# Kernel tuning notes

Measured on AMD Instinct MI355X. Metric: run time of the kernel, lower is better.

The kernel has to match this reference:

```python
import jax, jax.numpy as jnp
import numpy as np

N_NODES = 50000
N_EDGES = 300000
NODE_DIM = 128
HIDDEN = 256
BN_EPS = 1e-5
ROLL_SHIFT = 16


def setup_inputs() -> dict:
    key = jax.random.key(0)
    ks = jax.random.split(key, 8)
    node_feat = jax.random.normal(ks[0], (N_NODES, NODE_DIM), dtype=jnp.float32)
    edge_index = jax.random.randint(ks[1], (2, N_EDGES), 0, N_NODES, dtype=jnp.int64)
    W1 = jax.random.normal(ks[2], (2 * NODE_DIM, HIDDEN), dtype=jnp.float32) * 0.05
    b1 = jnp.zeros((HIDDEN,), dtype=jnp.float32)
    bn_gamma = jnp.ones((HIDDEN,), dtype=jnp.float32)
    bn_beta = jnp.zeros((HIDDEN,), dtype=jnp.float32)
    bn_mean = jax.random.normal(ks[3], (HIDDEN,), dtype=jnp.float32) * 0.1
    bn_var = jax.random.uniform(ks[4], (HIDDEN,), dtype=jnp.float32, minval=0.5, maxval=1.5)
    W2 = jax.random.normal(ks[5], (HIDDEN, 1), dtype=jnp.float32) * 0.05
    b2 = jnp.zeros((1,), dtype=jnp.float32)
    return {
        "node_feat": node_feat, "edge_index": edge_index,
        "W1": W1, "b1": b1,
        "bn_gamma": bn_gamma, "bn_beta": bn_beta,
        "bn_mean": bn_mean, "bn_var": bn_var,
        "W2": W2, "b2": b2,
    }


def reference(node_feat, edge_index, W1, b1, bn_gamma, bn_beta, bn_mean, bn_var, W2, b2):
    row, col = edge_index[0], edge_index[1]
    # [E, 2*node_dim]: gather endpoint features and concat
    edge_feat = jnp.concatenate([node_feat[row], node_feat[col]], axis=1)

    def mlp(x):
        h = x @ W1 + b1                                   # [E, H]
        # BatchNorm1d (eval mode: running stats)
        h = (h - bn_mean) * jax.lax.rsqrt(bn_var + BN_EPS) * bn_gamma + bn_beta
        h = jax.nn.relu(h)
        return (h @ W2 + b2).reshape(-1)                  # [E]

    edge_pred_1 = mlp(edge_feat)
    edge_pred_2 = mlp(jnp.roll(edge_feat, ROLL_SHIFT, axis=1))
    return jax.nn.sigmoid((edge_pred_1 + edge_pred_2) * 0.5)
```

## Files before the change

### kernel.cpp

```cpp
#include <hip/hip_runtime.h>
#include <hip/hip_bf16.h>

#define E_TOTAL 300000
#define N_NODES 50000
#define NDIM    128
#define KDIM    256
#define HDIM    512
#define BN_EPS  1e-5f
#define NTILES  ((E_TOTAL + 63) / 64)
#define NBLK    512
#define TLANES  512
#define NF_BLOCKS 6250
#define LT_MAX  10
#define A_SCALE 24.0f
#define WV_SCALE 16777216.0f
#define WV_INV   (1.0f / 16777216.0f)

typedef __attribute__((ext_vector_type(4))) int   i32x4;
typedef __attribute__((ext_vector_type(4))) float f32x4;
typedef _Float16 f16x2 __attribute__((ext_vector_type(2)));
typedef const __attribute__((address_space(1))) unsigned int* gas1_t;
typedef __attribute__((address_space(3))) unsigned int* las3_t;

__device__ __forceinline__ int q8(float x, float s) {
  float v = fminf(fmaxf(x * s, -127.f), 127.f);
  return (int)rintf(v);
}

__global__ void prep_kernel(const float* __restrict__ nf, unsigned char* __restrict__ nfq,
                            const float* __restrict__ W1, const float* __restrict__ b1,
                            const float* __restrict__ gamma, const float* __restrict__ beta,
                            const float* __restrict__ mean, const float* __restrict__ var,
                            const float* __restrict__ W2,
                            unsigned char* __restrict__ Wswz,
                            int* __restrict__ c2i, float* __restrict__ wp2) {
  int b = blockIdx.x;
  int tid = threadIdx.x;
  if (b < NF_BLOCKS) {
    int i = b * 256 + tid;
    float4 v = ((const float4*)nf)[i];
    int q0 = q8(v.x, A_SCALE), q1 = q8(v.y, A_SCALE);
    int q2 = q8(v.z, A_SCALE), q3 = q8(v.w, A_SCALE);
    ((unsigned*)nfq)[i] = (q0 & 255) | ((q1 & 255) << 8) | ((q2 & 255) << 16) | ((q3 & 255) << 24);
  } else {
    int ct = b - NF_BLOCKS;
    __shared__ float amx[16][16];
    __shared__ float sB[16];
    {
      int cl = tid >> 4, pt = tid & 15;
      int jj = (ct * 16 + cl) & 255;
      float m = 0.f;
      #pragma unroll
      for (int i = 0; i < 16; i++)
        m = fmaxf(m, fabsf(W1[(pt * 16 + i) * 256 + jj]));
      amx[cl][pt] = m;
    }
    __syncthreads();
    if (tid < 16) {
      int j  = ct * 16 + tid;
      int jj = j & 255;
      float s = gamma[jj] * rsqrtf(var[jj] + BN_EPS);
      float m = 0.f;
      #pragma unroll
      for (int p = 0; p < 16; p++) m = fmaxf(m, amx[tid][p]);
      float amax_b = fmaxf(m * fabsf(s), 1e-20f);
      sB[tid] = 127.f / amax_b;
      float rv = amax_b / (127.f * A_SCALE);
      float cj = b1[jj] * s + beta[jj] - mean[jj] * s;
      float c2 = fminf(fmaxf(cj / rv, -1e9f), 1e9f);
      c2i[j] = (int)rintf(c2);
      wp2[j] = 0.5f * W2[jj] * rv * WV_SCALE;
    }
    __syncthreads();
    {
      int kt   = tid >> 6;
      int lane = tid & 63;
      int l16  = lane & 15, quad = lane >> 4;
      int col  = ct * 16 + l16;
      int jj   = col & 255;
      int shift = (col >= 256) ? 16 : 0;
      float s  = gamma[jj] * rsqrtf(var[jj] + BN_EPS);
      float sc = sB[l16];
      unsigned o[4];
      #pragma unroll
      for (int d = 0; d < 4; d++) {
        unsigned pk = 0;
        #pragma unroll
        for (int jb = 0; jb < 4; jb++) {
          int k  = kt * 64 + quad * 16 + d * 4 + jb;
          int ks = (k + shift) & 255;
          int q  = q8(W1[ks * 256 + jj] * s, sc);
          pk |= (unsigned)(q & 255) << (8 * jb);
        }
        o[d] = pk;
      }
      *(uint4*)(Wswz + ((size_t)(ct * 4 + kt) * 64 + lane) * 16) = *(const uint4*)o;
    }
  }
}

__global__ __launch_bounds__(512, 4) void edge_mlp_kernel(
    const unsigned char* __restrict__ nfq, const int* __restrict__ eidx,
    const unsigned char* __restrict__ Wswz, const int* __restrict__ c2i,
    const float* __restrict__ wp2, const float* __restrict__ b2,
    float* __restrict__ out) {
  __shared__ unsigned char Ab[4][16 * 1024];
  __shared__ unsigned short idxl[LT_MAX * 128];
  __shared__ float partial[4][8][64];
  __shared__ int   c2il[HDIM];

  const int tid  = threadIdx.x;
  const int w    = tid >> 6;
  const int lane = tid & 63;
  const int l16  = lane & 15;
  const int quad = lane >> 4;
  const int tb   = blockIdx.x;
  const int ntl  = (NTILES - tb + TLANES - 1) / TLANES;

  const i32x4* Wf = (const i32x4*)Wswz;
  i32x4 bq[4][4];
  #pragma unroll
  for (int mt = 0; mt < 4; mt++)
    #pragma unroll
    for (int kt = 0; kt < 4; kt++)
      bq[mt][kt] = Wf[((w * 4 + mt) * 4 + kt) * 64 + lane];

  c2il[tid] = c2i[tid];
  f16x2 wvh[8];
  #pragma unroll
  for (int mt = 0; mt < 4; mt++) {
    float4 wvf = *(const float4*)&wp2[w * 64 + mt * 16 + quad * 4];
    wvh[mt * 2 + 0] = f16x2{(_Float16)wvf.x, (_Float16)wvf.y};
    wvh[mt * 2 + 1] = f16x2{(_Float16)wvf.z, (_Float16)wvf.w};
  }
  const float b2v = b2[0];

  for (int g = tid; g < ntl * 128; g += 512) {
    int lt2 = g >> 7, r = g & 127;
    int half = r >> 6;
    int e = (tb + lt2 * TLANES) * 64 + (r & 63);
    if (e >= E_TOTAL) e = E_TOTAL - 1;
    idxl[g] = (unsigned short)eidx[half * E_TOTAL + e];
  }
  __syncthreads();

  const int snt   = w & 3;
  const int shalf = w >> 2;
  const int sfrag0 = snt * 4 + shalf * 2;

  auto stage = [&](int lt2, int slot) {
    int node = idxl[lt2 * 128 + shalf * 64 + snt * 16 + l16];
    const unsigned char* gbase = nfq + (size_t)node * NDIM + quad * 16;
    #pragma unroll
    for (int i = 0; i < 2; i++)
      __builtin_amdgcn_global_load_lds((gas1_t)(gbase + i * 64),
                                       (las3_t)(&Ab[slot][(sfrag0 + i) * 1024]),
                                       16, 0, 0);
  };

  auto combine = [&](int lt2, int le) {
    int e = (tb + lt2 * TLANES) * 64 + le;
    if (e < E_TOTAL) {
      float s = 0.f;
      #pragma unroll
      for (int ww = 0; ww < 8; ww++) s += partial[lt2 & 3][ww][le];
      out[e] = 1.0f / (1.0f + __expf(-(s * WV_INV + b2v)));
    }
  };

  auto compute_tile = [&](int lt2) {
    const unsigned char* Ap = &Ab[lt2 & 3][lane * 16];

    #pragma unroll
    for (int nt = 0; nt < 4; nt++) {
      i32x4 acc[4];
      #pragma unroll
      for (int mt = 0; mt < 4; mt++)
        acc[mt] = *(const volatile i32x4*)&c2il[w * 64 + mt * 16 + quad * 4];
      #pragma unroll
      for (int kt = 0; kt < 4; kt++) {
        i32x4 ef = *(const i32x4*)(Ap + (nt * 4 + kt) * 1024);
        #pragma unroll
        for (int mt = 0; mt < 4; mt++)
          acc[mt] = __builtin_amdgcn_mfma_i32_16x16x64_i8(bq[mt][kt], ef, acc[mt], 0, 0, 0);
      }
      float v = 0.f;
      #pragma unroll
      for (int mt = 0; mt < 4; mt++) {
        int h;
        h = acc[mt][0]; v = fmaf((float)(h > 0 ? h : 0), (float)wvh[mt * 2 + 0][0], v);
        h = acc[mt][1]; v = fmaf((float)(h > 0 ? h : 0), (float)wvh[mt * 2 + 0][1], v);
        h = acc[mt][2]; v = fmaf((float)(h > 0 ? h : 0), (float)wvh[mt * 2 + 1][0], v);
        h = acc[mt][3]; v = fmaf((float)(h > 0 ? h : 0), (float)wvh[mt * 2 + 1][1], v);
      }
      v += __shfl_xor(v, 16);
      v += __shfl_xor(v, 32);
      if (quad == 0) partial[lt2 & 3][w][nt * 16 + l16] = v;
    }
  };

  stage(0, 0);
  if (1 < ntl) stage(1, 1);

  for (int lt = 0; lt < ntl; lt += 2) {
    __syncthreads();

    int s2 = lt + 2, s3 = lt + 3;
    if (s2 < ntl) stage(s2, s2 & 3);
    if (s3 < ntl) stage(s3, s3 & 3);

    if (lt >= 2) {
      if (tid < 64)       combine(lt - 2, tid);
      else if (tid < 128) combine(lt - 1, tid - 64);
    }

    compute_tile(lt);
    if (lt + 1 < ntl) compute_tile(lt + 1);
  }

  __syncthreads();
  if ((ntl & 1) == 0) {
    if (tid < 64)       combine(ntl - 2, tid);
    else if (tid < 128) combine(ntl - 1, tid - 64);
  } else {
    if (tid < 64)       combine(ntl - 1, tid);
  }
}

extern "C" void kernel_launch(void* const* d_in, const int* in_sizes, int n_in,
                              void* d_out, int out_size, void* d_ws, size_t ws_size,
                              hipStream_t stream) {
  const float* node_feat = (const float*)d_in[0];
  const int*   eidx      = (const int*)d_in[1];
  const float* W1        = (const float*)d_in[2];
  const float* b1        = (const float*)d_in[3];
  const float* gamma     = (const float*)d_in[4];
  const float* beta      = (const float*)d_in[5];
  const float* mean      = (const float*)d_in[6];
  const float* var       = (const float*)d_in[7];
  const float* W2        = (const float*)d_in[8];
  const float* b2        = (const float*)d_in[9];
  float* out = (float*)d_out;

  unsigned char* Wswz = (unsigned char*)d_ws;
  int*   c2i = (int*)((char*)d_ws + (size_t)HDIM * KDIM);
  float* wp2 = (float*)(c2i + HDIM);
  unsigned char* nfq = (unsigned char*)(wp2 + HDIM);

  prep_kernel<<<NF_BLOCKS + 32, 256, 0, stream>>>(node_feat, nfq, W1, b1, gamma, beta,
                                                  mean, var, W2, Wswz, c2i, wp2);

  edge_mlp_kernel<<<NBLK, 512, 0, stream>>>(nfq, eidx, Wswz, c2i, wp2, b2, out);
}
```

Measured before the change: 132.8 us.

## Fuse prep and edge MLP kernels with a grid-wide atomic barrier

Merges the quantization/weight-prep kernel into the edge MLP kernel. Blocks 0-31 build the swizzled int8 weights, staging W1 columns through shared memory, while the remaining blocks quantize node features in a grid-stride loop. A global atomic-counter barrier separates the prep phase from the compute phase, and the edge-index preload now runs before the barrier so it overlaps with prep. This removes one kernel launch and its tail, but adds a memset launch and relies on all 512 blocks being resident at once, otherwise the spin barrier deadlocks.

```diff
diff --git a/kernel.cpp b/kernel.cpp
--- a/kernel.cpp
+++ b/kernel.cpp
@@ -10,7 +10,7 @@
 #define NTILES  ((E_TOTAL + 63) / 64)
 #define NBLK    512
 #define TLANES  512
-#define NF_BLOCKS 6250
+#define NF4     (N_NODES * NDIM / 4)
 #define LT_MAX  10
 #define A_SCALE 24.0f
 #define WV_SCALE 16777216.0f
@@ -27,83 +27,15 @@
   return (int)rintf(v);
 }
 
-__global__ void prep_kernel(const float* __restrict__ nf, unsigned char* __restrict__ nfq,
-                            const float* __restrict__ W1, const float* __restrict__ b1,
-                            const float* __restrict__ gamma, const float* __restrict__ beta,
-                            const float* __restrict__ mean, const float* __restrict__ var,
-                            const float* __restrict__ W2,
-                            unsigned char* __restrict__ Wswz,
-                            int* __restrict__ c2i, float* __restrict__ wp2) {
-  int b = blockIdx.x;
-  int tid = threadIdx.x;
-  if (b < NF_BLOCKS) {
-    int i = b * 256 + tid;
-    float4 v = ((const float4*)nf)[i];
-    int q0 = q8(v.x, A_SCALE), q1 = q8(v.y, A_SCALE);
-    int q2 = q8(v.z, A_SCALE), q3 = q8(v.w, A_SCALE);
-    ((unsigned*)nfq)[i] = (q0 & 255) | ((q1 & 255) << 8) | ((q2 & 255) << 16) | ((q3 & 255) << 24);
-  } else {
-    int ct = b - NF_BLOCKS;
-    __shared__ float amx[16][16];
-    __shared__ float sB[16];
-    {
-      int cl = tid >> 4, pt = tid & 15;
-      int jj = (ct * 16 + cl) & 255;
-      float m = 0.f;
-      #pragma unroll
-      for (int i = 0; i < 16; i++)
-        m = fmaxf(m, fabsf(W1[(pt * 16 + i) * 256 + jj]));
-      amx[cl][pt] = m;
-    }
-    __syncthreads();
-    if (tid < 16) {
-      int j  = ct * 16 + tid;
-      int jj = j & 255;
-      float s = gamma[jj] * rsqrtf(var[jj] + BN_EPS);
-      float m = 0.f;
-      #pragma unroll
-      for (int p = 0; p < 16; p++) m = fmaxf(m, amx[tid][p]);
-      float amax_b = fmaxf(m * fabsf(s), 1e-20f);
-      sB[tid] = 127.f / amax_b;
-      float rv = amax_b / (127.f * A_SCALE);
-      float cj = b1[jj] * s + beta[jj] - mean[jj] * s;
-      float c2 = fminf(fmaxf(cj / rv, -1e9f), 1e9f);
-      c2i[j] = (int)rintf(c2);
-      wp2[j] = 0.5f * W2[jj] * rv * WV_SCALE;
-    }
-    __syncthreads();
-    {
-      int kt   = tid >> 6;
-      int lane = tid & 63;
-      int l16  = lane & 15, quad = lane >> 4;
-      int col  = ct * 16 + l16;
-      int jj   = col & 255;
-      int shift = (col >= 256) ? 16 : 0;
-      float s  = gamma[jj] * rsqrtf(var[jj] + BN_EPS);
-      float sc = sB[l16];
-      unsigned o[4];
-      #pragma unroll
-      for (int d = 0; d < 4; d++) {
-        unsigned pk = 0;
-        #pragma unroll
-        for (int jb = 0; jb < 4; jb++) {
-          int k  = kt * 64 + quad * 16 + d * 4 + jb;
-          int ks = (k + shift) & 255;
-          int q  = q8(W1[ks * 256 + jj] * s, sc);
-          pk |= (unsigned)(q & 255) << (8 * jb);
-        }
-        o[d] = pk;
-      }
-      *(uint4*)(Wswz + ((size_t)(ct * 4 + kt) * 64 + lane) * 16) = *(const uint4*)o;
-    }
-  }
-}
-
-__global__ __launch_bounds__(512, 4) void edge_mlp_kernel(
-    const unsigned char* __restrict__ nfq, const int* __restrict__ eidx,
-    const unsigned char* __restrict__ Wswz, const int* __restrict__ c2i,
-    const float* __restrict__ wp2, const float* __restrict__ b2,
-    float* __restrict__ out) {
+__global__ __launch_bounds__(512, 4) void fused_kernel(
+    const float* __restrict__ nf, const int* __restrict__ eidx,
+    const float* __restrict__ W1, const float* __restrict__ b1,
+    const float* __restrict__ gamma, const float* __restrict__ beta,
+    const float* __restrict__ mean, const float* __restrict__ var,
+    const float* __restrict__ W2, const float* __restrict__ b2,
+    unsigned char* __restrict__ Wswz, int* __restrict__ c2i,
+    float* __restrict__ wp2, unsigned char* __restrict__ nfq,
+    unsigned* __restrict__ bar, float* __restrict__ out) {
   __shared__ unsigned char Ab[4][16 * 1024];
   __shared__ unsigned short idxl[LT_MAX * 128];
   __shared__ float partial[4][8][64];
@@ -117,6 +49,98 @@
   const int tb   = blockIdx.x;
   const int ntl  = (NTILES - tb + TLANES - 1) / TLANES;
 
+  if (tb >= 32) {
+    const float4* nf4 = (const float4*)nf;
+    unsigned* nq4 = (unsigned*)nfq;
+    for (int i = (tb - 32) * 512 + tid; i < NF4; i += 480 * 512) {
+      float4 v = nf4[i];
+      int q0 = q8(v.x, A_SCALE), q1 = q8(v.y, A_SCALE);
+      int q2 = q8(v.z, A_SCALE), q3 = q8(v.w, A_SCALE);
+      nq4[i] = (q0 & 255) | ((q1 & 255) << 8) | ((q2 & 255) << 16) | ((q3 & 255) << 24);
+    }
+  } else {
+    int ct = tb;
+    float* wbuf = (float*)&Ab[0][0];
+    float* amx2 = (float*)&Ab[1][0];
+    float* sBl  = amx2 + 512;
+    {
+      const float4* src = (const float4*)(W1 + (ct & 15) * 16);
+      float4* dst = (float4*)wbuf;
+      #pragma unroll
+      for (int q = 0; q < 2; q++) {
+        int idx = q * 512 + tid;
+        int r = idx >> 2, c4 = idx & 3;
+        dst[idx] = src[(size_t)r * 64 + c4];
+      }
+    }
+    __syncthreads();
+    {
+      int col = tid & 15, chunk = tid >> 4;
+      float m = 0.f;
+      #pragma unroll
+      for (int i = 0; i < 8; i++)
+        m = fmaxf(m, fabsf(wbuf[(chunk * 8 + i) * 16 + col]));
+      amx2[col * 32 + chunk] = m;
+    }
+    __syncthreads();
+    if (tid < 16) {
+      int j  = ct * 16 + tid;
+      int jj = j & 255;
+      float s = gamma[jj] * rsqrtf(var[jj] + BN_EPS);
+      float m = 0.f;
+      #pragma unroll
+      for (int p = 0; p < 32; p++) m = fmaxf(m, amx2[tid * 32 + p]);
+      float amax_b = fmaxf(m * fabsf(s), 1e-20f);
+      sBl[tid] = 127.f / amax_b;
+      float rv = amax_b / (127.f * A_SCALE);
+      float cj = b1[jj] * s + beta[jj] - mean[jj] * s;
+      float c2 = fminf(fmaxf(cj / rv, -1e9f), 1e9f);
+      c2i[j] = (int)rintf(c2);
+      wp2[j] = 0.5f * W2[jj] * rv * WV_SCALE;
+    }
+    __syncthreads();
+    if (tid < 256) {
+      int kt = tid >> 6, ln = tid & 63;
+      int lc = ln & 15, qd = ln >> 4;
+      int col = ct * 16 + lc;
+      int jj  = col & 255;
+      int shift = (col >= 256) ? 16 : 0;
+      float s  = gamma[jj] * rsqrtf(var[jj] + BN_EPS);
+      float sc = sBl[lc];
+      unsigned o[4];
+      #pragma unroll
+      for (int d = 0; d < 4; d++) {
+        unsigned pk = 0;
+        #pragma unroll
+        for (int jb = 0; jb < 4; jb++) {
+          int k  = kt * 64 + qd * 16 + d * 4 + jb;
+          int ks = (k + shift) & 255;
+          int q  = q8(wbuf[ks * 16 + lc] * s, sc);
+          pk |= (unsigned)(q & 255) << (8 * jb);
+        }
+        o[d] = pk;
+      }
+      *(uint4*)(Wswz + ((size_t)(ct * 4 + kt) * 64 + ln) * 16) = *(const uint4*)o;
+    }
+  }
+
+  for (int g = tid; g < ntl * 128; g += 512) {
+    int lt2 = g >> 7, r = g & 127;
+    int half = r >> 6;
+    int e = (tb + lt2 * TLANES) * 64 + (r & 63);
+    if (e >= E_TOTAL) e = E_TOTAL - 1;
+    idxl[g] = (unsigned short)eidx[half * E_TOTAL + e];
+  }
+
+  __syncthreads();
+  __threadfence();
+  if (tid == 0) {
+    atomicAdd(bar, 1u);
+    while (atomicAdd(bar, 0u) < NBLK) __builtin_amdgcn_s_sleep(8);
+    __threadfence();
+  }
+  __syncthreads();
+
   const i32x4* Wf = (const i32x4*)Wswz;
   i32x4 bq[4][4];
   #pragma unroll
@@ -134,15 +158,6 @@
     wvh[mt * 2 + 1] = f16x2{(_Float16)wvf.z, (_Float16)wvf.w};
   }
   const float b2v = b2[0];
-
-  for (int g = tid; g < ntl * 128; g += 512) {
-    int lt2 = g >> 7, r = g & 127;
-    int half = r >> 6;
-    int e = (tb + lt2 * TLANES) * 64 + (r & 63);
-    if (e >= E_TOTAL) e = E_TOTAL - 1;
-    idxl[g] = (unsigned short)eidx[half * E_TOTAL + e];
-  }
-  __syncthreads();
 
   const int snt   = w & 3;
   const int shalf = w >> 2;
@@ -246,9 +261,11 @@
   int*   c2i = (int*)((char*)d_ws + (size_t)HDIM * KDIM);
   float* wp2 = (float*)(c2i + HDIM);
   unsigned char* nfq = (unsigned char*)(wp2 + HDIM);
-
-  prep_kernel<<<NF_BLOCKS + 32, 256, 0, stream>>>(node_feat, nfq, W1, b1, gamma, beta,
-                                                  mean, var, W2, Wswz, c2i, wp2);
-
-  edge_mlp_kernel<<<NBLK, 512, 0, stream>>>(nfq, eidx, Wswz, c2i, wp2, b2, out);
+  unsigned* bar = (unsigned*)(nfq + (size_t)N_NODES * NDIM);
+
+  hipMemsetAsync(bar, 0, sizeof(unsigned), stream);
+
+  fused_kernel<<<NBLK, 512, 0, stream>>>(node_feat, eidx, W1, b1, gamma, beta,
+                                         mean, var, W2, b2,
+                                         Wswz, c2i, wp2, nfq, bar, out);
 }
```

New measurement: 211.6 us. +59.4%, slower.

## Split hidden dimension across two blocks per edge tile with separate sigmoid pass

Applied to the files above, without the earlier changes.

Each edge tile is now handled by two 256-thread blocks, each covering one half of the 512 hidden units (the two rolled MLP passes). Each block writes a partial dot product to workspace, and a new small kernel sums the two halves and applies the sigmoid. The pipeline drops from 4-slot double-tile staging to a simple 2-slot ring, which cuts LDS use per block and should allow more resident blocks and smaller scheduling units. In exchange every node row is gathered twice, there is an extra kernel launch, and partial sums make a round trip through global memory.

```diff
diff --git a/kernel.cpp b/kernel.cpp
--- a/kernel.cpp
+++ b/kernel.cpp
@@ -8,7 +8,7 @@
 #define HDIM    512
 #define BN_EPS  1e-5f
 #define NTILES  ((E_TOTAL + 63) / 64)
-#define NBLK    512
+#define NBLK    1024
 #define TLANES  512
 #define NF_BLOCKS 6250
 #define LT_MAX  10
@@ -17,7 +17,6 @@
 #define WV_INV   (1.0f / 16777216.0f)
 
 typedef __attribute__((ext_vector_type(4))) int   i32x4;
-typedef __attribute__((ext_vector_type(4))) float f32x4;
 typedef _Float16 f16x2 __attribute__((ext_vector_type(2)));
 typedef const __attribute__((address_space(1))) unsigned int* gas1_t;
 typedef __attribute__((address_space(3))) unsigned int* las3_t;
@@ -99,22 +98,23 @@
   }
 }
 
-__global__ __launch_bounds__(512, 4) void edge_mlp_kernel(
+__global__ __launch_bounds__(256, 4) void edge_mlp_kernel(
     const unsigned char* __restrict__ nfq, const int* __restrict__ eidx,
     const unsigned char* __restrict__ Wswz, const int* __restrict__ c2i,
-    const float* __restrict__ wp2, const float* __restrict__ b2,
-    float* __restrict__ out) {
-  __shared__ unsigned char Ab[4][16 * 1024];
+    const float* __restrict__ wp2, float* __restrict__ part) {
+  __shared__ unsigned char Ab[2][16 * 1024];
   __shared__ unsigned short idxl[LT_MAX * 128];
-  __shared__ float partial[4][8][64];
-  __shared__ int   c2il[HDIM];
+  __shared__ float partial[2][4][64];
+  __shared__ int   c2il[256];
 
   const int tid  = threadIdx.x;
   const int w    = tid >> 6;
   const int lane = tid & 63;
   const int l16  = lane & 15;
   const int quad = lane >> 4;
-  const int tb   = blockIdx.x;
+  const int b    = blockIdx.x;
+  const int ph   = b & 1;
+  const int tb   = b >> 1;
   const int ntl  = (NTILES - tb + TLANES - 1) / TLANES;
 
   const i32x4* Wf = (const i32x4*)Wswz;
@@ -123,19 +123,18 @@
   for (int mt = 0; mt < 4; mt++)
     #pragma unroll
     for (int kt = 0; kt < 4; kt++)
-      bq[mt][kt] = Wf[((w * 4 + mt) * 4 + kt) * 64 + lane];
-
-  c2il[tid] = c2i[tid];
+      bq[mt][kt] = Wf[(((ph * 16 + w * 4 + mt) * 4) + kt) * 64 + lane];
+
+  c2il[tid] = c2i[ph * 256 + tid];
   f16x2 wvh[8];
   #pragma unroll
   for (int mt = 0; mt < 4; mt++) {
-    float4 wvf = *(const float4*)&wp2[w * 64 + mt * 16 + quad * 4];
+    float4 wvf = *(const float4*)&wp2[ph * 256 + w * 64 + mt * 16 + quad * 4];
     wvh[mt * 2 + 0] = f16x2{(_Float16)wvf.x, (_Float16)wvf.y};
     wvh[mt * 2 + 1] = f16x2{(_Float16)wvf.z, (_Float16)wvf.w};
   }
-  const float b2v = b2[0];
-
-  for (int g = tid; g < ntl * 128; g += 512) {
+
+  for (int g = tid; g < ntl * 128; g += 256) {
     int lt2 = g >> 7, r = g & 127;
     int half = r >> 6;
     int e = (tb + lt2 * TLANES) * 64 + (r & 63);
@@ -144,18 +143,20 @@
   }
   __syncthreads();
 
-  const int snt   = w & 3;
-  const int shalf = w >> 2;
-  const int sfrag0 = snt * 4 + shalf * 2;
-
   auto stage = [&](int lt2, int slot) {
-    int node = idxl[lt2 * 128 + shalf * 64 + snt * 16 + l16];
-    const unsigned char* gbase = nfq + (size_t)node * NDIM + quad * 16;
+    int node_r = idxl[lt2 * 128 + w * 16 + l16];
+    int node_c = idxl[lt2 * 128 + 64 + w * 16 + l16];
+    const unsigned char* gr = nfq + (size_t)node_r * NDIM + quad * 16;
+    const unsigned char* gc = nfq + (size_t)node_c * NDIM + quad * 16;
     #pragma unroll
-    for (int i = 0; i < 2; i++)
-      __builtin_amdgcn_global_load_lds((gas1_t)(gbase + i * 64),
-                                       (las3_t)(&Ab[slot][(sfrag0 + i) * 1024]),
+    for (int i = 0; i < 2; i++) {
+      __builtin_amdgcn_global_load_lds((gas1_t)(gr + i * 64),
+                                       (las3_t)(&Ab[slot][(w * 4 + i) * 1024]),
                                        16, 0, 0);
+      __builtin_amdgcn_global_load_lds((gas1_t)(gc + i * 64),
+                                       (las3_t)(&Ab[slot][(w * 4 + 2 + i) * 1024]),
+                                       16, 0, 0);
+    }
   };
 
   auto combine = [&](int lt2, int le) {
@@ -163,13 +164,13 @@
     if (e < E_TOTAL) {
       float s = 0.f;
       #pragma unroll
-      for (int ww = 0; ww < 8; ww++) s += partial[lt2 & 3][ww][le];
-      out[e] = 1.0f / (1.0f + __expf(-(s * WV_INV + b2v)));
+      for (int ww = 0; ww < 4; ww++) s += partial[lt2 & 1][ww][le];
+      part[ph * E_TOTAL + e] = s;
     }
   };
 
   auto compute_tile = [&](int lt2) {
-    const unsigned char* Ap = &Ab[lt2 & 3][lane * 16];
+    const unsigned char* Ap = &Ab[lt2 & 1][lane * 16];
 
     #pragma unroll
     for (int nt = 0; nt < 4; nt++) {
@@ -195,35 +196,40 @@
       }
       v += __shfl_xor(v, 16);
       v += __shfl_xor(v, 32);
-      if (quad == 0) partial[lt2 & 3][w][nt * 16 + l16] = v;
+      if (quad == 0) partial[lt2 & 1][w][nt * 16 + l16] = v;
     }
   };
 
   stage(0, 0);
-  if (1 < ntl) stage(1, 1);
-
-  for (int lt = 0; lt < ntl; lt += 2) {
+
+  for (int lt = 0; lt < ntl; lt++) {
     __syncthreads();
 
-    int s2 = lt + 2, s3 = lt + 3;
-    if (s2 < ntl) stage(s2, s2 & 3);
-    if (s3 < ntl) stage(s3, s3 & 3);
-
-    if (lt >= 2) {
-      if (tid < 64)       combine(lt - 2, tid);
-      else if (tid < 128) combine(lt - 1, tid - 64);
-    }
+    if (lt + 1 < ntl) stage(lt + 1, (lt + 1) & 1);
+
+    if (lt >= 1 && tid < 64) combine(lt - 1, tid);
 
     compute_tile(lt);
-    if (lt + 1 < ntl) compute_tile(lt + 1);
   }
 
   __syncthreads();
-  if ((ntl & 1) == 0) {
-    if (tid < 64)       combine(ntl - 2, tid);
-    else if (tid < 128) combine(ntl - 1, tid - 64);
-  } else {
-    if (tid < 64)       combine(ntl - 1, tid);
+  if (tid < 64) combine(ntl - 1, tid);
+}
+
+__global__ void sigmoid_kernel(const float* __restrict__ part,
+                               const float* __restrict__ b2,
+                               float* __restrict__ out) {
+  int i = blockIdx.x * 256 + threadIdx.x;
+  if (i < E_TOTAL / 4) {
+    float4 a = ((const float4*)part)[i];
+    float4 c = ((const float4*)(part + E_TOTAL))[i];
+    float bb = b2[0];
+    float4 o;
+    o.x = 1.0f / (1.0f + __expf(-((a.x + c.x) * WV_INV + bb)));
+    o.y = 1.0f / (1.0f + __expf(-((a.y + c.y) * WV_INV + bb)));
+    o.z = 1.0f / (1.0f + __expf(-((a.z + c.z) * WV_INV + bb)));
+    o.w = 1.0f / (1.0f + __expf(-((a.w + c.w) * WV_INV + bb)));
+    ((float4*)out)[i] = o;
   }
 }
 
@@ -246,9 +252,12 @@
   int*   c2i = (int*)((char*)d_ws + (size_t)HDIM * KDIM);
   float* wp2 = (float*)(c2i + HDIM);
   unsigned char* nfq = (unsigned char*)(wp2 + HDIM);
+  float* part = (float*)(nfq + (size_t)N_NODES * NDIM);
 
   prep_kernel<<<NF_BLOCKS + 32, 256, 0, stream>>>(node_feat, nfq, W1, b1, gamma, beta,
                                                   mean, var, W2, Wswz, c2i, wp2);
 
-  edge_mlp_kernel<<<NBLK, 512, 0, stream>>>(nfq, eidx, Wswz, c2i, wp2, b2, out);
-}
+  edge_mlp_kernel<<<NBLK, 256, 0, stream>>>(nfq, eidx, Wswz, c2i, wp2, part);
+
+  sigmoid_kernel<<<(E_TOTAL / 4 + 255) / 256, 256, 0, stream>>>(part, b2, out);
+}
```

Result: slower. 140.7 us (+5.9%).
